# Performance work log

Measured on AMD Instinct MI355X. Metric: run time of the kernel, lower is better.

The kernel has to match this reference:

```python
import jax, jax.numpy as jnp
import numpy as np

B, N, F_DIM, HID, HEADS = 4, 1024, 512, 64, 8  # feature_dim == HID*HEADS required by the module's += broadcast


def setup_inputs() -> dict:
    key = jax.random.key(0)
    ks = jax.random.split(key, 16)
    s = 0.05
    return {
        'node_features_a': jax.random.normal(ks[0], (B, N, F_DIM), dtype=jnp.float32),
        'node_features_b': jax.random.normal(ks[1], (B, N, F_DIM), dtype=jnp.float32),
        'A_intra_a': jax.random.uniform(ks[2], (B, N, N), dtype=jnp.float32),
        'A_intra_b': jax.random.uniform(ks[3], (B, N, N), dtype=jnp.float32),
        'A_inter': jax.random.uniform(ks[4], (B, N, N), dtype=jnp.float32),
        # stacked per-head Linear weights (torch ModuleList F1/F2/F3), [H, F, K]
        'W1': jax.random.normal(ks[5], (HEADS, F_DIM, HID), dtype=jnp.float32) * s,
        'b1': jnp.zeros((HEADS, HID), jnp.float32),
        'W2': jax.random.normal(ks[6], (HEADS, F_DIM, HID), dtype=jnp.float32) * s,
        'b2': jnp.zeros((HEADS, HID), jnp.float32),
        'W3': jax.random.normal(ks[7], (HEADS, F_DIM, HID), dtype=jnp.float32) * s,
        'b3': jnp.zeros((HEADS, HID), jnp.float32),
        'W_intra_a': jax.random.normal(ks[8], (HID, HID), dtype=jnp.float32) * s,
        'W_intra_b': jax.random.normal(ks[9], (HID, HID), dtype=jnp.float32) * s,
        'W_inter': jax.random.normal(ks[10], (HID, HID), dtype=jnp.float32) * s,
        'W_out': jax.random.normal(ks[11], (F_DIM, HID * HEADS), dtype=jnp.float32) * s,  # torch Linear weight [out,in]
        'b_out': jnp.zeros((F_DIM,), jnp.float32),
        'b_output': jnp.zeros((F_DIM,), jnp.float32),
    }


def _aggregate(src, tgt, adj, ew, W1, b1, W2, b2, W3, b3, W_out, b_out, b_output):
    # per-head projections, batched over heads instead of a Python loop
    F1u = jnp.einsum('bnf,hfk->bhnk', src, W1) + b1[:, None, :]
    F2v = jnp.einsum('bmf,hfk->bhmk', tgt, W2) + b2[:, None, :]
    F3u = jnp.einsum('bnf,hfk->bhnk', src, W3) + b3[:, None, :]
    # attention_scores = F1_u @ (edge_weight @ F2_v^T)  -> [B,H,N,N]
    scores = jnp.einsum('bhnk,kl,bhml->bhnm', F1u, ew, F2v)
    # multiplicative adjacency mask, then softmax over last dim
    attn = jax.nn.softmax(scores * adj[:, None, :, :], axis=-1)
    msgs = jnp.einsum('bhnm,bhmk->bhnk', attn, F3u)
    b_, h_, n_, k_ = msgs.shape
    concat = msgs.transpose(0, 2, 1, 3).reshape(b_, n_, h_ * k_)  # cat heads on last dim
    return jax.nn.relu(concat @ W_out.T + b_out) + b_output


def reference(node_features_a, node_features_b, A_intra_a, A_intra_b, A_inter,
              W1, b1, W2, b2, W3, b3, W_intra_a, W_intra_b, W_inter,
              W_out, b_out, b_output):
    p = (W1, b1, W2, b2, W3, b3)
    o = (W_out, b_out, b_output)
    ua = _aggregate(node_features_a, node_features_a, A_intra_a, W_intra_a, *p, *o)
    ub = _aggregate(node_features_b, node_features_b, A_intra_b, W_intra_b, *p, *o)
    ia = _aggregate(node_features_a, node_features_b, A_inter, W_inter, *p, *o)
    ib = _aggregate(node_features_b, node_features_a, jnp.swapaxes(A_inter, 1, 2), W_inter, *p, *o)
    return (ua + ia, ub + ib)
```

## Files before the change

kernel.cpp:

```cpp
#include <hip/hip_runtime.h>
#include <hip/hip_bf16.h>

#define BB 4
#define NN 1024
#define FF 512
#define HH 8
#define KK 64
#define PSZ ((size_t)BB * HH * NN * KK)

#define XAOFF 0u
#define XBOFF 2097152u
#define WTOFF 4194304u
#define WOOFF (WTOFF + 786432u)
#define PBOFF (WOOFF + 262144u)
#define MSOFF (PBOFF + 6u * 2097152u)
#define ADOFF (MSOFF + 4u * 2097152u)
#define ADSZ  4194304u

#define LOG2E 1.4426950408889634f
#define SHIFT2 34.624683f

typedef unsigned short u16;
typedef __attribute__((ext_vector_type(8))) short bf16x8;
typedef __attribute__((ext_vector_type(4))) short bf16x4;
typedef __attribute__((ext_vector_type(4))) float f32x4;
typedef __attribute__((ext_vector_type(8))) unsigned short ushort8;
typedef __attribute__((ext_vector_type(4))) unsigned short ushort4v;

#if defined(__has_builtin)
#if __has_builtin(__builtin_amdgcn_mfma_f32_16x16x16bf16_1k)
#define HAVE_MFMA16 1
#endif
#if __has_builtin(__builtin_amdgcn_global_load_lds)
#define HAVE_GLL 1
#endif
#endif
#ifndef HAVE_MFMA16
#define HAVE_MFMA16 0
#endif
#ifndef HAVE_GLL
#define HAVE_GLL 0
#endif

#if HAVE_GLL
#define GSTR 64
#else
#define GSTR 72
#endif

__device__ __forceinline__ u16 f2b(float x) {
    union { float f; unsigned u; } v; v.f = x;
    unsigned r = v.u + 0x7FFF + ((v.u >> 16) & 1);
    return (u16)(r >> 16);
}
__device__ __forceinline__ float b2f(u16 x) {
    union { unsigned u; float f; } v; v.u = ((unsigned)x) << 16;
    return v.f;
}

__global__ __launch_bounds__(256) void prep_kernel(
    const float* __restrict__ Xa, const float* __restrict__ Xb,
    const float* __restrict__ Wout,
    const float* __restrict__ W1, const float* __restrict__ W2,
    const float* __restrict__ W3,
    u16* __restrict__ ws)
{
    __shared__ float T[64][65];
    const int bid = blockIdx.x;
    const int t = threadIdx.x;

    if (bid < 192) {
        const int j  = bid / 64;
        const int rem = bid & 63;
        const int h  = rem >> 3;
        const int f0 = (rem & 7) * 64;
        const float* Wj = j == 0 ? W1 : (j == 1 ? W2 : W3);
        const int tr = t >> 2, tc = (t & 3) * 16;
        const float* src = Wj + (size_t)h * FF * KK + (size_t)(f0 + tr) * KK + tc;
        #pragma unroll
        for (int jj = 0; jj < 4; ++jj) {
            float4 v = *(const float4*)(src + 4 * jj);
            T[tr][tc + 4 * jj + 0] = v.x;
            T[tr][tc + 4 * jj + 1] = v.y;
            T[tr][tc + 4 * jj + 2] = v.z;
            T[tr][tc + 4 * jj + 3] = v.w;
        }
        __syncthreads();
        ushort8 w0, w1;
        #pragma unroll
        for (int jj = 0; jj < 8; ++jj) {
            w0[jj] = f2b(T[tc + jj][tr]);
            w1[jj] = f2b(T[tc + 8 + jj][tr]);
        }
        u16* d = ws + WTOFF + (unsigned)j * 262144u + (unsigned)(h * 64 + tr) * 512u + f0 + tc;
        *(ushort8*)&d[0] = w0;
        *(ushort8*)&d[8] = w1;
        return;
    }

    const int NFLAT4 = (2097152 + 2097152 + 262144) / 4;
    const int nb = gridDim.x - 192;
    for (int idx = (bid - 192) * 256 + t; idx < NFLAT4; idx += nb * 256) {
        int e = idx * 4;
        const float* src; u16* dst;
        if (e < 2097152)      { src = Xa + e;             dst = ws + XAOFF + e; }
        else if (e < 4194304) { src = Xb + (e - 2097152); dst = ws + XBOFF + (e - 2097152); }
        else                  { src = Wout + (e - 4194304); dst = ws + WOOFF + (e - 4194304); }
        float4 v = *(const float4*)src;
        ushort4v w;
        w[0] = f2b(v.x); w[1] = f2b(v.y); w[2] = f2b(v.z); w[3] = f2b(v.w);
        *(ushort4v*)dst = w;
    }
}

__global__ __launch_bounds__(256) void perm_kernel(
    const float* __restrict__ Aia, const float* __restrict__ Aib,
    const float* __restrict__ Ain, u16* __restrict__ ws)
{
    const int z = blockIdx.z;
    const int b = blockIdx.y;
    const int x = blockIdx.x;
    const int qblk = x >> 4, mt = x & 15;
    const float* A = (z == 0 ? Aia : (z == 1 ? Aib : Ain)) + ((size_t)b << 20);
    u16* out = ws + ADOFF + (size_t)z * ADSZ + ((size_t)b << 20) + (size_t)x * 8192;
    const int t = threadIdx.x;
    const int w = t >> 6, l = t & 63;
    const int lg = l >> 4, li = l & 15;
    #pragma unroll
    for (int u = 0; u < 2; ++u)
        #pragma unroll
        for (int t_ = 0; t_ < 4; ++t_) {
            const int row = qblk * 128 + w * 32 + u * 16 + li;
            const int col = mt * 64 + t_ * 16 + lg * 4;
            float4 v = *(const float4*)&A[(size_t)row * NN + col];
            ushort4v o;
            o[0] = f2b(v.x * LOG2E); o[1] = f2b(v.y * LOG2E);
            o[2] = f2b(v.z * LOG2E); o[3] = f2b(v.w * LOG2E);
            *(ushort4v*)&out[(size_t)(w * 8 + u * 4 + t_) * 256 + l * 4] = o;
        }
}

__global__ __launch_bounds__(256) void permt_kernel(const float* __restrict__ Ain, u16* __restrict__ dst)
{
    const int b = blockIdx.y;
    const int x = blockIdx.x;
    const int qblk = x >> 4, mt = x & 15;
    __shared__ float T[64][132];
    const int t = threadIdx.x;
    const int tr = t >> 2, tc = (t & 3) * 32;
    const float* src = Ain + ((size_t)b << 20) + (size_t)(mt * 64 + tr) * NN + qblk * 128 + tc;
    #pragma unroll
    for (int j = 0; j < 8; ++j) {
        float4 v = *(const float4*)(src + 4 * j);
        T[tr][tc + 4 * j + 0] = v.x;
        T[tr][tc + 4 * j + 1] = v.y;
        T[tr][tc + 4 * j + 2] = v.z;
        T[tr][tc + 4 * j + 3] = v.w;
    }
    __syncthreads();
    const int w = t >> 6, l = t & 63;
    const int lg = l >> 4, li = l & 15;
    u16* out = dst + ((size_t)b << 20) + (size_t)x * 8192;
    #pragma unroll
    for (int u = 0; u < 2; ++u)
        #pragma unroll
        for (int t_ = 0; t_ < 4; ++t_) {
            ushort4v o;
            #pragma unroll
            for (int e = 0; e < 4; ++e)
                o[e] = f2b(T[t_ * 16 + lg * 4 + e][w * 32 + u * 16 + li] * LOG2E);
            *(ushort4v*)&out[(size_t)(w * 8 + u * 4 + t_) * 256 + l * 4] = o;
        }
}

__global__ __launch_bounds__(256) void proj_kernel(
    const float* __restrict__ b1v, const float* __restrict__ b2v,
    const float* __restrict__ b3v,
    u16* __restrict__ ws)
{
    const int z  = blockIdx.z;
    const int src = z / 3, pj = z % 3;
    const u16* X  = ws + (src ? XBOFF : XAOFF);
    const u16* Wt = ws + WTOFF + (unsigned)pj * 262144u;
    const float* bias = pj == 0 ? b1v : (pj == 1 ? b2v : b3v);
    u16* P = ws + PBOFF + (size_t)z * PSZ;

    const int rb = blockIdx.y * 128;
    const int cb = blockIdx.x * 128;
    const int t  = threadIdx.x;
    const int lane = t & 63, wave = t >> 6;
    const int lg = lane >> 4, li = lane & 15;
    const int wr = wave >> 1, wc = wave & 1;

    __shared__ u16 As[128 * GSTR];
    __shared__ u16 Bs[128 * GSTR];

    f32x4 acc[4][4];
    #pragma unroll
    for (int m = 0; m < 4; ++m)
        #pragma unroll
        for (int n = 0; n < 4; ++n) acc[m][n] = (f32x4){0.f, 0.f, 0.f, 0.f};

#if !HAVE_GLL
    const int srow = t >> 1, sf0 = (t & 1) * 32;
#endif

    for (int fb = 0; fb < FF; fb += 64) {
        __syncthreads();
#if HAVE_GLL
        {
            const int gr = wave * 32 + (lane >> 3);
            const int gc = (lane & 7) * 8;
            #pragma unroll
            for (int i = 0; i < 4; ++i) {
                __builtin_amdgcn_global_load_lds(
                    (const unsigned int*)&X[(size_t)(rb + gr + 8 * i) * FF + fb + gc],
                    (unsigned int*)&As[(wave * 32 + 8 * i) * GSTR], 16, 0, 0);
                __builtin_amdgcn_global_load_lds(
                    (const unsigned int*)&Wt[(size_t)(cb + gr + 8 * i) * FF + fb + gc],
                    (unsigned int*)&Bs[(wave * 32 + 8 * i) * GSTR], 16, 0, 0);
            }
        }
#else
        #pragma unroll
        for (int s = 0; s < 4; ++s) {
            *(ushort8*)&As[srow * GSTR + sf0 + 8 * s] =
                *(const ushort8*)&X[(size_t)(rb + srow) * FF + fb + sf0 + 8 * s];
            *(ushort8*)&Bs[srow * GSTR + sf0 + 8 * s] =
                *(const ushort8*)&Wt[(size_t)(cb + srow) * FF + fb + sf0 + 8 * s];
        }
#endif
        __syncthreads();

        bf16x8 af[4][2], bf[4][2];
        #pragma unroll
        for (int m = 0; m < 4; ++m) {
            af[m][0] = *(const bf16x8*)&As[(wr * 64 + m * 16 + li) * GSTR + 8 * lg];
            af[m][1] = *(const bf16x8*)&As[(wr * 64 + m * 16 + li) * GSTR + 8 * lg + 32];
        }
        #pragma unroll
        for (int n = 0; n < 4; ++n) {
            bf[n][0] = *(const bf16x8*)&Bs[(wc * 64 + n * 16 + li) * GSTR + 8 * lg];
            bf[n][1] = *(const bf16x8*)&Bs[(wc * 64 + n * 16 + li) * GSTR + 8 * lg + 32];
        }
        #pragma unroll
        for (int m = 0; m < 4; ++m)
            #pragma unroll
            for (int n = 0; n < 4; ++n) {
                acc[m][n] = __builtin_amdgcn_mfma_f32_16x16x32_bf16(af[m][0], bf[n][0], acc[m][n], 0, 0, 0);
                acc[m][n] = __builtin_amdgcn_mfma_f32_16x16x32_bf16(af[m][1], bf[n][1], acc[m][n], 0, 0, 0);
            }
    }

    if (pj != 2) {
        #pragma unroll
        for (int m = 0; m < 4; ++m)
            #pragma unroll
            for (int n = 0; n < 4; ++n)
                #pragma unroll
                for (int r = 0; r < 4; ++r) {
                    int row = rb + wr * 64 + m * 16 + 4 * lg + r;
                    int col = cb + wc * 64 + n * 16 + li;
                    int b_ = row >> 10, n_ = row & 1023;
                    int h = col >> 6, k = col & 63;
                    P[((size_t)(b_ * HH + h) * NN + n_) * KK + k] = f2b(acc[m][n][r] + bias[col]);
                }
    } else {
        #pragma unroll
        for (int m = 0; m < 4; ++m)
            #pragma unroll
            for (int n = 0; n < 4; ++n) {
                int col = cb + wc * 64 + n * 16 + li;
                int h = col >> 6, k = col & 63;
                int row0 = rb + wr * 64 + m * 16 + 4 * lg;
                int b_ = row0 >> 10, n0 = row0 & 1023;
                float bsv = bias[col];
                ushort4v w;
                #pragma unroll
                for (int r = 0; r < 4; ++r) w[r] = f2b(acc[m][n][r] + bsv);
                *(ushort4v*)&P[((size_t)(b_ * HH + h) * KK + k) * NN + n0] = w;
            }
    }
}

#define SWU(ROW, CU) (((ROW) << 6) + ((CU) ^ (((ROW) & 7) << 3)))

__global__ __launch_bounds__(256, 4) void attn_kernel(
    const u16* __restrict__ Pbase,
    const float* __restrict__ Wia, const float* __restrict__ Wib, const float* __restrict__ Win,
    const u16* __restrict__ AD, const u16* __restrict__ AinT,
    u16* __restrict__ msgs)
{
    const int flat = blockIdx.x;
    const int lf   = (flat & 7) * 128 + (flat >> 3);
    const int qblk = lf & 7;
    const int qb   = qblk * 128;
    const int bh   = (lf >> 3) & 31;
    const int agg  = lf >> 8;
    const int b = bh >> 3, h = bh & 7;
    const int t = threadIdx.x;
    const int lane = t & 63, wave = t >> 6;
    const int lg = lane >> 4, li = lane & 15;

    const u16 *Qp, *Kp, *Vp, *adjp; const float* ew;
    switch (agg) {
      case 0: Qp = Pbase;         ew = Wia; Kp = Pbase + 1*PSZ; Vp = Pbase + 2*PSZ; adjp = AD;          break;
      case 1: Qp = Pbase + 3*PSZ; ew = Wib; Kp = Pbase + 4*PSZ; Vp = Pbase + 5*PSZ; adjp = AD + 1*ADSZ; break;
      case 2: Qp = Pbase;         ew = Win; Kp = Pbase + 4*PSZ; Vp = Pbase + 2*PSZ; adjp = AD + 2*ADSZ; break;
      default:Qp = Pbase + 3*PSZ; ew = Win; Kp = Pbase + 1*PSZ; Vp = Pbase + 5*PSZ; adjp = AinT;        break;
    }
    const size_t bhoff = (size_t)(b * HH + h) * NN * KK;
    const u16* Qbh  = Qp + bhoff;
    const u16* Kbh  = Kp + bhoff;
    const u16* Vbh  = Vp + bhoff;
    const u16* advs = adjp + ((size_t)b << 20) + (size_t)qblk * 131072u
                           + (unsigned)(wave * 2048 + lane * 4);

    __shared__ u16 SM[16384];
    u16* preQ = SM;
    u16* preF = SM + 8192;
    u16* preE = SM + 12288;

    const int sr  = t >> 2;
    const int sc  = (t & 3) * 16;

    #pragma unroll
    for (int j = 0; j < 16; ++j)
        preE[SWU(sc + j, sr)] = f2b(ew[sr * 64 + sc + j]);

    #pragma unroll
    for (int p = 0; p < 2; ++p) {
        __syncthreads();
        {
            const ushort8* src = (const ushort8*)&Qbh[(size_t)(qb + p * 64 + sr) * KK + sc];
            *(ushort8*)&preF[SWU(sr, sc)]     = src[0];
            *(ushort8*)&preF[SWU(sr, sc + 8)] = src[1];
        }
        __syncthreads();
        bf16x8 a0 = *(const bf16x8*)&preF[SWU(wave * 16 + li, 8 * lg)];
        bf16x8 a1 = *(const bf16x8*)&preF[SWU(wave * 16 + li, 8 * lg + 32)];
        #pragma unroll
        for (int t_ = 0; t_ < 4; ++t_) {
            bf16x8 b0 = *(const bf16x8*)&preE[SWU(li + 16 * t_, 8 * lg)];
            bf16x8 b1 = *(const bf16x8*)&preE[SWU(li + 16 * t_, 8 * lg + 32)];
            f32x4 q = {0.f, 0.f, 0.f, 0.f};
            q = __builtin_amdgcn_mfma_f32_16x16x32_bf16(a0, b0, q, 0, 0, 0);
            q = __builtin_amdgcn_mfma_f32_16x16x32_bf16(a1, b1, q, 0, 0, 0);
            #pragma unroll
            for (int r = 0; r < 4; ++r)
                preQ[SWU(p * 64 + wave * 16 + 4 * lg + r, li + 16 * t_)] = f2b(q[r]);
        }
    }
    __syncthreads();
    bf16x8 qB[2][2];
    #pragma unroll
    for (int u = 0; u < 2; ++u)
        #pragma unroll
        for (int c = 0; c < 2; ++c)
            qB[u][c] = *(const bf16x8*)&preQ[SWU(wave * 32 + u * 16 + li, 32 * c + 8 * lg)];
    __syncthreads();

    f32x4 oacc[2][4];
    #pragma unroll
    for (int u = 0; u < 2; ++u)
        #pragma unroll
        for (int f_ = 0; f_ < 4; ++f_) oacc[u][f_] = (f32x4){0.f, 0.f, 0.f, 0.f};
    float lsum[2] = {0.f, 0.f};

#if HAVE_MFMA16
    {
        const ushort8* ks = (const ushort8*)&Kbh[(size_t)sr * KK + sc];
        *(ushort8*)&SM[SWU(sr, sc)]            = ks[0];
        *(ushort8*)&SM[SWU(sr, sc + 8)]        = ks[1];
        const ushort8* vs = (const ushort8*)&Vbh[(size_t)sr * NN + sc];
        *(ushort8*)&SM[8192 + SWU(sr, sc)]     = vs[0];
        *(ushort8*)&SM[8192 + SWU(sr, sc + 8)] = vs[1];
    }
    __syncthreads();

    for (int mt = 0; mt < 16; ++mt) {
        const int cur = (mt & 1) * 4096;
        const u16* Kc = SM + cur;
        const u16* Vc = SM + 8192 + cur;

        ushort8 kr0, kr1, vr0, vr1;
        if (mt < 15) {
            const int mb2 = (mt + 1) * 64;
            const ushort8* ks = (const ushort8*)&Kbh[(size_t)(mb2 + sr) * KK + sc];
            kr0 = ks[0]; kr1 = ks[1];
            const ushort8* vs = (const ushort8*)&Vbh[(size_t)sr * NN + mb2 + sc];
            vr0 = vs[0]; vr1 = vs[1];
        }

        ushort4v adv[2][4];
        {
            const u16* ap = advs + (size_t)mt * 8192;
            #pragma unroll
            for (int u = 0; u < 2; ++u)
                #pragma unroll
                for (int t_ = 0; t_ < 4; ++t_)
                    adv[u][t_] = *(const ushort4v*)&ap[(u * 4 + t_) * 256];
        }

        bf16x4 pa[2][4];
        #pragma unroll
        for (int t_ = 0; t_ < 4; ++t_) {
            bf16x8 kb0 = *(const bf16x8*)&Kc[SWU(li + 16 * t_, 8 * lg)];
            bf16x8 kb1 = *(const bf16x8*)&Kc[SWU(li + 16 * t_, 8 * lg + 32)];
            #pragma unroll
            for (int u = 0; u < 2; ++u) {
                f32x4 s = {0.f, 0.f, 0.f, 0.f};
                __builtin_amdgcn_s_setprio(1);
                s = __builtin_amdgcn_mfma_f32_16x16x32_bf16(kb0, qB[u][0], s, 0, 0, 0);
                s = __builtin_amdgcn_mfma_f32_16x16x32_bf16(kb1, qB[u][1], s, 0, 0, 0);
                __builtin_amdgcn_s_setprio(0);
                float p0 = __builtin_amdgcn_exp2f(fmaf(s[0], b2f(adv[u][t_][0]), -SHIFT2));
                float p1 = __builtin_amdgcn_exp2f(fmaf(s[1], b2f(adv[u][t_][1]), -SHIFT2));
                float p2 = __builtin_amdgcn_exp2f(fmaf(s[2], b2f(adv[u][t_][2]), -SHIFT2));
                float p3 = __builtin_amdgcn_exp2f(fmaf(s[3], b2f(adv[u][t_][3]), -SHIFT2));
                lsum[u] += (p0 + p1) + (p2 + p3);
                unsigned w0, w1;
                asm("v_cvt_pk_bf16_f32 %0, %1, %2" : "=v"(w0) : "v"(p0), "v"(p1));
                asm("v_cvt_pk_bf16_f32 %0, %1, %2" : "=v"(w1) : "v"(p2), "v"(p3));
                union { uint2 u2; bf16x4 v; } pk;
                pk.u2.x = w0; pk.u2.y = w1;
                pa[u][t_] = pk.v;
            }
        }

        __builtin_amdgcn_s_setprio(1);
        #pragma unroll
        for (int f_ = 0; f_ < 4; ++f_) {
            #pragma unroll
            for (int t_ = 0; t_ < 4; ++t_) {
                bf16x4 vb = *(const bf16x4*)&Vc[SWU(li + 16 * f_, 16 * t_ + 4 * lg)];
                oacc[0][f_] = __builtin_amdgcn_mfma_f32_16x16x16bf16_1k(pa[0][t_], vb, oacc[0][f_], 0, 0, 0);
                oacc[1][f_] = __builtin_amdgcn_mfma_f32_16x16x16bf16_1k(pa[1][t_], vb, oacc[1][f_], 0, 0, 0);
            }
        }
        __builtin_amdgcn_s_setprio(0);

        if (mt < 15) {
            const int nxt = ((mt & 1) ^ 1) * 4096;
            *(ushort8*)&SM[nxt + SWU(sr, sc)]            = kr0;
            *(ushort8*)&SM[nxt + SWU(sr, sc + 8)]        = kr1;
            *(ushort8*)&SM[8192 + nxt + SWU(sr, sc)]     = vr0;
            *(ushort8*)&SM[8192 + nxt + SWU(sr, sc + 8)] = vr1;
        }
        __syncthreads();
    }
#else
    u16* Kt = SM;
    u16* Vt = SM + 4096;
    u16* Pq = SM + 8192;
    for (int mt = 0; mt < 16; ++mt) {
        const int mb = mt * 64;
        __syncthreads();
        {
            const ushort8* ks = (const ushort8*)&Kbh[(size_t)(mb + sr) * KK + sc];
            *(ushort8*)&Kt[SWU(sr, sc)]     = ks[0];
            *(ushort8*)&Kt[SWU(sr, sc + 8)] = ks[1];
            const ushort8* vs = (const ushort8*)&Vbh[(size_t)sr * NN + mb + sc];
            *(ushort8*)&Vt[SWU(sr, sc)]     = vs[0];
            *(ushort8*)&Vt[SWU(sr, sc + 8)] = vs[1];
        }
        __syncthreads();

        ushort4v adv[2][4];
        {
            const u16* ap = advs + (size_t)mt * 8192;
            #pragma unroll
            for (int u = 0; u < 2; ++u)
                #pragma unroll
                for (int t_ = 0; t_ < 4; ++t_)
                    adv[u][t_] = *(const ushort4v*)&ap[(u * 4 + t_) * 256];
        }

        #pragma unroll
        for (int t_ = 0; t_ < 4; ++t_) {
            bf16x8 kb0 = *(const bf16x8*)&Kt[SWU(li + 16 * t_, 8 * lg)];
            bf16x8 kb1 = *(const bf16x8*)&Kt[SWU(li + 16 * t_, 8 * lg + 32)];
            #pragma unroll
            for (int u = 0; u < 2; ++u) {
                f32x4 s = {0.f, 0.f, 0.f, 0.f};
                s = __builtin_amdgcn_mfma_f32_16x16x32_bf16(kb0, qB[u][0], s, 0, 0, 0);
                s = __builtin_amdgcn_mfma_f32_16x16x32_bf16(kb1, qB[u][1], s, 0, 0, 0);
                float p0 = __builtin_amdgcn_exp2f(fmaf(s[0], b2f(adv[u][t_][0]), -SHIFT2));
                float p1 = __builtin_amdgcn_exp2f(fmaf(s[1], b2f(adv[u][t_][1]), -SHIFT2));
                float p2 = __builtin_amdgcn_exp2f(fmaf(s[2], b2f(adv[u][t_][2]), -SHIFT2));
                float p3 = __builtin_amdgcn_exp2f(fmaf(s[3], b2f(adv[u][t_][3]), -SHIFT2));
                lsum[u] += (p0 + p1) + (p2 + p3);
                unsigned w0, w1;
                asm("v_cvt_pk_bf16_f32 %0, %1, %2" : "=v"(w0) : "v"(p0), "v"(p1));
                asm("v_cvt_pk_bf16_f32 %0, %1, %2" : "=v"(w1) : "v"(p2), "v"(p3));
                uint2 pd; pd.x = w0; pd.y = w1;
                *(uint2*)&Pq[SWU(wave * 32 + u * 16 + li, 16 * t_ + 4 * lg)] = pd;
            }
        }
        {
            bf16x8 pA[2][2];
            #pragma unroll
            for (int u = 0; u < 2; ++u) {
                pA[u][0] = *(const bf16x8*)&Pq[SWU(wave * 32 + u * 16 + li, 8 * lg)];
                pA[u][1] = *(const bf16x8*)&Pq[SWU(wave * 32 + u * 16 + li, 8 * lg + 32)];
            }
            #pragma unroll
            for (int f_ = 0; f_ < 4; ++f_) {
                bf16x8 vb0 = *(const bf16x8*)&Vt[SWU(li + 16 * f_, 8 * lg)];
                bf16x8 vb1 = *(const bf16x8*)&Vt[SWU(li + 16 * f_, 8 * lg + 32)];
                #pragma unroll
                for (int u = 0; u < 2; ++u) {
                    oacc[u][f_] = __builtin_amdgcn_mfma_f32_16x16x32_bf16(pA[u][0], vb0, oacc[u][f_], 0, 0, 0);
                    oacc[u][f_] = __builtin_amdgcn_mfma_f32_16x16x32_bf16(pA[u][1], vb1, oacc[u][f_], 0, 0, 0);
                }
            }
        }
    }
#endif

    #pragma unroll
    for (int u = 0; u < 2; ++u) {
        lsum[u] += __shfl_xor(lsum[u], 16);
        lsum[u] += __shfl_xor(lsum[u], 32);
    }
    #pragma unroll
    for (int u = 0; u < 2; ++u)
        #pragma unroll
        for (int r = 0; r < 4; ++r) {
            float inv = 1.f / __shfl(lsum[u], 4 * lg + r);
            int row = qb + wave * 32 + u * 16 + 4 * lg + r;
            u16* dst = msgs + (size_t)agg * PSZ + ((size_t)b * NN + row) * (HH * KK) + h * KK;
            #pragma unroll
            for (int f_ = 0; f_ < 4; ++f_)
                dst[li + 16 * f_] = f2b(oacc[u][f_][r] * inv);
        }
}

__global__ __launch_bounds__(256) void out_kernel(
    const u16* __restrict__ ws,
    const float* __restrict__ bo, const float* __restrict__ bo2,
    float* __restrict__ out)
{
    const int z  = blockIdx.z;
    const u16* M1 = ws + MSOFF + (size_t)z * PSZ;
    const u16* M2 = ws + MSOFF + (size_t)(2 + z) * PSZ;
    const u16* Wb = ws + WOOFF;
    const int rb = blockIdx.y * 64;
    const int cb = blockIdx.x * 128;
    const int t  = threadIdx.x;
    const int lane = t & 63, wave = t >> 6;
    const int lg = lane >> 4, li = lane & 15;
    const int wr = wave >> 1, wc = wave & 1;

    __shared__ u16 A1s[64 * GSTR];
    __shared__ u16 A2s[64 * GSTR];
    __shared__ u16 Bs[128 * GSTR];

    f32x4 acc1[2][4], acc2[2][4];
    #pragma unroll
    for (int m = 0; m < 2; ++m)
        #pragma unroll
        for (int n = 0; n < 4; ++n) {
            acc1[m][n] = (f32x4){0.f, 0.f, 0.f, 0.f};
            acc2[m][n] = (f32x4){0.f, 0.f, 0.f, 0.f};
        }

    for (int fb = 0; fb < FF; fb += 64) {
        __syncthreads();
#if HAVE_GLL
        {
            const int lr = lane >> 3;
            const int gc = (lane & 7) * 8;
            #pragma unroll
            for (int i = 0; i < 2; ++i) {
                __builtin_amdgcn_global_load_lds(
                    (const unsigned int*)&M1[(size_t)(rb + wave * 16 + 8 * i + lr) * FF + fb + gc],
                    (unsigned int*)&A1s[(wave * 16 + 8 * i) * GSTR], 16, 0, 0);
                __builtin_amdgcn_global_load_lds(
                    (const unsigned int*)&M2[(size_t)(rb + wave * 16 + 8 * i + lr) * FF + fb + gc],
                    (unsigned int*)&A2s[(wave * 16 + 8 * i) * GSTR], 16, 0, 0);
            }
            #pragma unroll
            for (int i = 0; i < 4; ++i) {
                __builtin_amdgcn_global_load_lds(
                    (const unsigned int*)&Wb[(size_t)(cb + wave * 32 + 8 * i + lr) * FF + fb + gc],
                    (unsigned int*)&Bs[(wave * 32 + 8 * i) * GSTR], 16, 0, 0);
            }
        }
#else
        {
            int ar = t >> 2, ac = (t & 3) * 16;
            *(ushort8*)&A1s[ar * GSTR + ac]     = *(const ushort8*)&M1[(size_t)(rb + ar) * FF + fb + ac];
            *(ushort8*)&A1s[ar * GSTR + ac + 8] = *(const ushort8*)&M1[(size_t)(rb + ar) * FF + fb + ac + 8];
            *(ushort8*)&A2s[ar * GSTR + ac]     = *(const ushort8*)&M2[(size_t)(rb + ar) * FF + fb + ac];
            *(ushort8*)&A2s[ar * GSTR + ac + 8] = *(const ushort8*)&M2[(size_t)(rb + ar) * FF + fb + ac + 8];
            int br = t >> 1, bc = (t & 1) * 32;
            #pragma unroll
            for (int s = 0; s < 4; ++s)
                *(ushort8*)&Bs[br * GSTR + bc + 8 * s] =
                    *(const ushort8*)&Wb[(size_t)(cb + br) * FF + fb + bc + 8 * s];
        }
#endif
        __syncthreads();

        #pragma unroll
        for (int m = 0; m < 2; ++m) {
            bf16x8 a10 = *(const bf16x8*)&A1s[(wr * 32 + m * 16 + li) * GSTR + 8 * lg];
            bf16x8 a11 = *(const bf16x8*)&A1s[(wr * 32 + m * 16 + li) * GSTR + 8 * lg + 32];
            bf16x8 a20 = *(const bf16x8*)&A2s[(wr * 32 + m * 16 + li) * GSTR + 8 * lg];
            bf16x8 a21 = *(const bf16x8*)&A2s[(wr * 32 + m * 16 + li) * GSTR + 8 * lg + 32];
            #pragma unroll
            for (int n = 0; n < 4; ++n) {
                bf16x8 b0 = *(const bf16x8*)&Bs[(wc * 64 + n * 16 + li) * GSTR + 8 * lg];
                bf16x8 b1 = *(const bf16x8*)&Bs[(wc * 64 + n * 16 + li) * GSTR + 8 * lg + 32];
                acc1[m][n] = __builtin_amdgcn_mfma_f32_16x16x32_bf16(a10, b0, acc1[m][n], 0, 0, 0);
                acc1[m][n] = __builtin_amdgcn_mfma_f32_16x16x32_bf16(a11, b1, acc1[m][n], 0, 0, 0);
                acc2[m][n] = __builtin_amdgcn_mfma_f32_16x16x32_bf16(a20, b0, acc2[m][n], 0, 0, 0);
                acc2[m][n] = __builtin_amdgcn_mfma_f32_16x16x32_bf16(a21, b1, acc2[m][n], 0, 0, 0);
            }
        }
    }

    #pragma unroll
    for (int m = 0; m < 2; ++m)
        #pragma unroll
        for (int n = 0; n < 4; ++n)
            #pragma unroll
            for (int r = 0; r < 4; ++r) {
                int row = rb + wr * 32 + m * 16 + 4 * lg + r;
                int col = cb + wc * 64 + n * 16 + li;
                float v1 = fmaxf(acc1[m][n][r] + bo[col], 0.f);
                float v2 = fmaxf(acc2[m][n][r] + bo[col], 0.f);
                out[(size_t)z * (BB * NN * FF) + (size_t)row * FF + col] = v1 + v2 + 2.f * bo2[col];
            }
}

extern "C" void kernel_launch(void* const* d_in, const int* in_sizes, int n_in,
                              void* d_out, int out_size, void* d_ws, size_t ws_size,
                              hipStream_t stream) {
    const float* nfa  = (const float*)d_in[0];
    const float* nfb  = (const float*)d_in[1];
    const float* Aia  = (const float*)d_in[2];
    const float* Aib  = (const float*)d_in[3];
    const float* Ain  = (const float*)d_in[4];
    const float* W1   = (const float*)d_in[5];
    const float* b1   = (const float*)d_in[6];
    const float* W2   = (const float*)d_in[7];
    const float* b2   = (const float*)d_in[8];
    const float* W3   = (const float*)d_in[9];
    const float* b3   = (const float*)d_in[10];
    const float* Wia  = (const float*)d_in[11];
    const float* Wib  = (const float*)d_in[12];
    const float* Win  = (const float*)d_in[13];
    const float* Wout = (const float*)d_in[14];
    const float* bo   = (const float*)d_in[15];
    const float* bo2  = (const float*)d_in[16];

    u16* ws = (u16*)d_ws;
    float* out = (float*)d_out;

    prep_kernel<<<1536, 256, 0, stream>>>(nfa, nfb, Wout, W1, W2, W3, ws);
    perm_kernel<<<dim3(128, 4, 3), 256, 0, stream>>>(Aia, Aib, Ain, ws);
    proj_kernel<<<dim3(4, 32, 6), 256, 0, stream>>>(b1, b2, b3, ws);
    permt_kernel<<<dim3(128, 4), 256, 0, stream>>>(Ain, ws + XAOFF);
    attn_kernel<<<1024, 256, 0, stream>>>(ws + PBOFF, Wia, Wib, Win, ws + ADOFF, ws + XAOFF, ws + MSOFF);
    out_kernel<<<dim3(4, 64, 2), 256, 0, stream>>>(ws, bo, bo2, out);
}
```

Measured before the change: 133.6 us.

## Split attention key dimension across wave pairs and stage K/V via global_load_lds

```diff
diff --git a/kernel.cpp b/kernel.cpp
--- a/kernel.cpp
+++ b/kernel.cpp
@@ -285,7 +285,7 @@
 
 #define SWU(ROW, CU) (((ROW) << 6) + ((CU) ^ (((ROW) & 7) << 3)))
 
-__global__ __launch_bounds__(256, 4) void attn_kernel(
+__global__ __launch_bounds__(512, 6) void attn_kernel(
     const u16* __restrict__ Pbase,
     const float* __restrict__ Wia, const float* __restrict__ Wib, const float* __restrict__ Win,
     const u16* __restrict__ AD, const u16* __restrict__ AinT,
@@ -301,6 +301,7 @@
     const int t = threadIdx.x;
     const int lane = t & 63, wave = t >> 6;
     const int lg = lane >> 4, li = lane & 15;
+    const int qg = wave >> 1, mh = wave & 1;
 
     const u16 *Qp, *Kp, *Vp, *adjp; const float* ew;
     switch (agg) {
@@ -314,31 +315,30 @@
     const u16* Kbh  = Kp + bhoff;
     const u16* Vbh  = Vp + bhoff;
     const u16* advs = adjp + ((size_t)b << 20) + (size_t)qblk * 131072u
-                           + (unsigned)(wave * 2048 + lane * 4);
+                           + (unsigned)((qg * 8 + mh * 2) * 256 + lane * 4);
 
     __shared__ u16 SM[16384];
-    u16* preQ = SM;
-    u16* preF = SM + 8192;
-    u16* preE = SM + 12288;
-
-    const int sr  = t >> 2;
-    const int sc  = (t & 3) * 16;
-
-    #pragma unroll
-    for (int j = 0; j < 16; ++j)
-        preE[SWU(sc + j, sr)] = f2b(ew[sr * 64 + sc + j]);
-
-    #pragma unroll
-    for (int p = 0; p < 2; ++p) {
-        __syncthreads();
-        {
-            const ushort8* src = (const ushort8*)&Qbh[(size_t)(qb + p * 64 + sr) * KK + sc];
-            *(ushort8*)&preF[SWU(sr, sc)]     = src[0];
-            *(ushort8*)&preF[SWU(sr, sc + 8)] = src[1];
-        }
-        __syncthreads();
-        bf16x8 a0 = *(const bf16x8*)&preF[SWU(wave * 16 + li, 8 * lg)];
-        bf16x8 a1 = *(const bf16x8*)&preF[SWU(wave * 16 + li, 8 * lg + 32)];
+    char* SMc = (char*)SM;
+    u16* Qs   = SM;
+    u16* preE = SM + 8192;
+
+    {
+        const int sr3 = t >> 3, sc3 = (t & 7) * 8;
+        #pragma unroll
+        for (int j = 0; j < 8; ++j)
+            preE[SWU(sc3 + j, sr3)] = f2b(ew[sr3 * 64 + sc3 + j]);
+    }
+    {
+        const int qr = t >> 2, qc = (t & 3) * 16;
+        const ushort8* src = (const ushort8*)&Qbh[(size_t)(qb + qr) * KK + qc];
+        *(ushort8*)&Qs[SWU(qr, qc)]     = src[0];
+        *(ushort8*)&Qs[SWU(qr, qc + 8)] = src[1];
+    }
+    __syncthreads();
+    f32x4 qreg[4];
+    {
+        bf16x8 a0 = *(const bf16x8*)&Qs[SWU(wave * 16 + li, 8 * lg)];
+        bf16x8 a1 = *(const bf16x8*)&Qs[SWU(wave * 16 + li, 8 * lg + 32)];
         #pragma unroll
         for (int t_ = 0; t_ < 4; ++t_) {
             bf16x8 b0 = *(const bf16x8*)&preE[SWU(li + 16 * t_, 8 * lg)];
@@ -346,18 +346,22 @@
             f32x4 q = {0.f, 0.f, 0.f, 0.f};
             q = __builtin_amdgcn_mfma_f32_16x16x32_bf16(a0, b0, q, 0, 0, 0);
             q = __builtin_amdgcn_mfma_f32_16x16x32_bf16(a1, b1, q, 0, 0, 0);
-            #pragma unroll
-            for (int r = 0; r < 4; ++r)
-                preQ[SWU(p * 64 + wave * 16 + 4 * lg + r, li + 16 * t_)] = f2b(q[r]);
-        }
-    }
+            qreg[t_] = q;
+        }
+    }
+    __syncthreads();
+    #pragma unroll
+    for (int t_ = 0; t_ < 4; ++t_)
+        #pragma unroll
+        for (int r = 0; r < 4; ++r)
+            Qs[SWU(wave * 16 + 4 * lg + r, li + 16 * t_)] = f2b(qreg[t_][r]);
     __syncthreads();
     bf16x8 qB[2][2];
     #pragma unroll
     for (int u = 0; u < 2; ++u)
         #pragma unroll
         for (int c = 0; c < 2; ++c)
-            qB[u][c] = *(const bf16x8*)&preQ[SWU(wave * 32 + u * 16 + li, 32 * c + 8 * lg)];
+            qB[u][c] = *(const bf16x8*)&Qs[SWU(qg * 32 + u * 16 + li, 32 * c + 8 * lg)];
     __syncthreads();
 
     f32x4 oacc[2][4];
@@ -367,44 +371,47 @@
         for (int f_ = 0; f_ < 4; ++f_) oacc[u][f_] = (f32x4){0.f, 0.f, 0.f, 0.f};
     float lsum[2] = {0.f, 0.f};
 
-#if HAVE_MFMA16
-    {
-        const ushort8* ks = (const ushort8*)&Kbh[(size_t)sr * KK + sc];
-        *(ushort8*)&SM[SWU(sr, sc)]            = ks[0];
-        *(ushort8*)&SM[SWU(sr, sc + 8)]        = ks[1];
-        const ushort8* vs = (const ushort8*)&Vbh[(size_t)sr * NN + sc];
-        *(ushort8*)&SM[8192 + SWU(sr, sc)]     = vs[0];
-        *(ushort8*)&SM[8192 + SWU(sr, sc + 8)] = vs[1];
-    }
+#if HAVE_MFMA16 && HAVE_GLL
+    const int lrow = lane >> 3;
+    const int lcs  = ((lane & 7) ^ lrow) * 8;
+
+    __builtin_amdgcn_global_load_lds(
+        (const unsigned int*)&Kbh[(size_t)(wave * 8 + lrow) * KK + lcs],
+        (unsigned int*)(SMc + wave * 1024), 16, 0, 0);
+    __builtin_amdgcn_global_load_lds(
+        (const unsigned int*)&Vbh[(size_t)(wave * 8 + lrow) * NN + lcs],
+        (unsigned int*)(SMc + 16384 + wave * 1024), 16, 0, 0);
     __syncthreads();
 
     for (int mt = 0; mt < 16; ++mt) {
-        const int cur = (mt & 1) * 4096;
-        const u16* Kc = SM + cur;
-        const u16* Vc = SM + 8192 + cur;
-
-        ushort8 kr0, kr1, vr0, vr1;
+        const u16* Kc = (const u16*)(SMc + (mt & 1) * 8192);
+        const u16* Vc = (const u16*)(SMc + 16384 + (mt & 1) * 8192);
+
         if (mt < 15) {
             const int mb2 = (mt + 1) * 64;
-            const ushort8* ks = (const ushort8*)&Kbh[(size_t)(mb2 + sr) * KK + sc];
-            kr0 = ks[0]; kr1 = ks[1];
-            const ushort8* vs = (const ushort8*)&Vbh[(size_t)sr * NN + mb2 + sc];
-            vr0 = vs[0]; vr1 = vs[1];
-        }
-
-        ushort4v adv[2][4];
+            const int nb  = ((mt & 1) ^ 1) * 8192;
+            __builtin_amdgcn_global_load_lds(
+                (const unsigned int*)&Kbh[(size_t)(mb2 + wave * 8 + lrow) * KK + lcs],
+                (unsigned int*)(SMc + nb + wave * 1024), 16, 0, 0);
+            __builtin_amdgcn_global_load_lds(
+                (const unsigned int*)&Vbh[(size_t)(wave * 8 + lrow) * NN + mb2 + lcs],
+                (unsigned int*)(SMc + 16384 + nb + wave * 1024), 16, 0, 0);
+        }
+
+        ushort4v adv[2][2];
         {
             const u16* ap = advs + (size_t)mt * 8192;
             #pragma unroll
             for (int u = 0; u < 2; ++u)
                 #pragma unroll
-                for (int t_ = 0; t_ < 4; ++t_)
-                    adv[u][t_] = *(const ushort4v*)&ap[(u * 4 + t_) * 256];
-        }
-
-        bf16x4 pa[2][4];
-        #pragma unroll
-        for (int t_ = 0; t_ < 4; ++t_) {
+                for (int tt = 0; tt < 2; ++tt)
+                    adv[u][tt] = *(const ushort4v*)&ap[(u * 4 + tt) * 256];
+        }
+
+        bf16x4 pa[2][2];
+        #pragma unroll
+        for (int tt = 0; tt < 2; ++tt) {
+            const int t_ = mh * 2 + tt;
             bf16x8 kb0 = *(const bf16x8*)&Kc[SWU(li + 16 * t_, 8 * lg)];
             bf16x8 kb1 = *(const bf16x8*)&Kc[SWU(li + 16 * t_, 8 * lg + 32)];
             #pragma unroll
@@ -414,17 +421,17 @@
                 s = __builtin_amdgcn_mfma_f32_16x16x32_bf16(kb0, qB[u][0], s, 0, 0, 0);
                 s = __builtin_amdgcn_mfma_f32_16x16x32_bf16(kb1, qB[u][1], s, 0, 0, 0);
                 __builtin_amdgcn_s_setprio(0);
-                float p0 = __builtin_amdgcn_exp2f(fmaf(s[0], b2f(adv[u][t_][0]), -SHIFT2));
-                float p1 = __builtin_amdgcn_exp2f(fmaf(s[1], b2f(adv[u][t_][1]), -SHIFT2));
-                float p2 = __builtin_amdgcn_exp2f(fmaf(s[2], b2f(adv[u][t_][2]), -SHIFT2));
-                float p3 = __builtin_amdgcn_exp2f(fmaf(s[3], b2f(adv[u][t_][3]), -SHIFT2));
+                float p0 = __builtin_amdgcn_exp2f(fmaf(s[0], b2f(adv[u][tt][0]), -SHIFT2));
+                float p1 = __builtin_amdgcn_exp2f(fmaf(s[1], b2f(adv[u][tt][1]), -SHIFT2));
+                float p2 = __builtin_amdgcn_exp2f(fmaf(s[2], b2f(adv[u][tt][2]), -SHIFT2));
+                float p3 = __builtin_amdgcn_exp2f(fmaf(s[3], b2f(adv[u][tt][3]), -SHIFT2));
                 lsum[u] += (p0 + p1) + (p2 + p3);
                 unsigned w0, w1;
                 asm("v_cvt_pk_bf16_f32 %0, %1, %2" : "=v"(w0) : "v"(p0), "v"(p1));
                 asm("v_cvt_pk_bf16_f32 %0, %1, %2" : "=v"(w1) : "v"(p2), "v"(p3));
                 union { uint2 u2; bf16x4 v; } pk;
                 pk.u2.x = w0; pk.u2.y = w1;
-                pa[u][t_] = pk.v;
+                pa[u][tt] = pk.v;
             }
         }
 
@@ -432,77 +439,108 @@
         #pragma unroll
         for (int f_ = 0; f_ < 4; ++f_) {
             #pragma unroll
-            for (int t_ = 0; t_ < 4; ++t_) {
+            for (int tt = 0; tt < 2; ++tt) {
+                const int t_ = mh * 2 + tt;
                 bf16x4 vb = *(const bf16x4*)&Vc[SWU(li + 16 * f_, 16 * t_ + 4 * lg)];
-                oacc[0][f_] = __builtin_amdgcn_mfma_f32_16x16x16bf16_1k(pa[0][t_], vb, oacc[0][f_], 0, 0, 0);
-                oacc[1][f_] = __builtin_amdgcn_mfma_f32_16x16x16bf16_1k(pa[1][t_], vb, oacc[1][f_], 0, 0, 0);
+                oacc[0][f_] = __builtin_amdgcn_mfma_f32_16x16x16bf16_1k(pa[0][tt], vb, oacc[0][f_], 0, 0, 0);
+                oacc[1][f_] = __builtin_amdgcn_mfma_f32_16x16x16bf16_1k(pa[1][tt], vb, oacc[1][f_], 0, 0, 0);
             }
         }
         __builtin_amdgcn_s_setprio(0);
 
-        if (mt < 15) {
-            const int nxt = ((mt & 1) ^ 1) * 4096;
-            *(ushort8*)&SM[nxt + SWU(sr, sc)]            = kr0;
-            *(ushort8*)&SM[nxt + SWU(sr, sc + 8)]        = kr1;
-            *(ushort8*)&SM[8192 + nxt + SWU(sr, sc)]     = vr0;
-            *(ushort8*)&SM[8192 + nxt + SWU(sr, sc + 8)] = vr1;
-        }
         __syncthreads();
+    }
+
+    #pragma unroll
+    for (int u = 0; u < 2; ++u) {
+        lsum[u] += __shfl_xor(lsum[u], 16);
+        lsum[u] += __shfl_xor(lsum[u], 32);
+    }
+    float* SMf = (float*)SM;
+    if (lg == 0) {
+        SMf[wave * 32 + li]      = lsum[0];
+        SMf[wave * 32 + 16 + li] = lsum[1];
+    }
+    __syncthreads();
+    #pragma unroll
+    for (int u = 0; u < 2; ++u)
+        lsum[u] = SMf[wave * 32 + u * 16 + li] + SMf[(wave ^ 1) * 32 + u * 16 + li];
+    __syncthreads();
+    if (mh == 0) {
+        #pragma unroll
+        for (int u = 0; u < 2; ++u)
+            #pragma unroll
+            for (int f_ = 0; f_ < 4; ++f_)
+                #pragma unroll
+                for (int r = 0; r < 4; ++r)
+                    SMf[qg * 2048 + (u * 16 + 4 * lg + r) * 64 + li + 16 * f_] = oacc[u][f_][r];
+    }
+    __syncthreads();
+    if (mh == 1) {
+        #pragma unroll
+        for (int u = 0; u < 2; ++u)
+            #pragma unroll
+            for (int r = 0; r < 4; ++r) {
+                float inv = 1.f / __shfl(lsum[u], 4 * lg + r);
+                int row = qb + qg * 32 + u * 16 + 4 * lg + r;
+                u16* dst = msgs + (size_t)agg * PSZ + ((size_t)b * NN + row) * (HH * KK) + h * KK;
+                #pragma unroll
+                for (int f_ = 0; f_ < 4; ++f_) {
+                    float v = oacc[u][f_][r]
+                            + SMf[qg * 2048 + (u * 16 + 4 * lg + r) * 64 + li + 16 * f_];
+                    dst[li + 16 * f_] = f2b(v * inv);
+                }
+            }
     }
 #else
     u16* Kt = SM;
     u16* Vt = SM + 4096;
     u16* Pq = SM + 8192;
+    const u16* apf = adjp + ((size_t)b << 20) + (size_t)qblk * 131072u
+                          + (unsigned)(qg * 8 * 256 + lane * 4);
     for (int mt = 0; mt < 16; ++mt) {
         const int mb = mt * 64;
         __syncthreads();
         {
-            const ushort8* ks = (const ushort8*)&Kbh[(size_t)(mb + sr) * KK + sc];
-            *(ushort8*)&Kt[SWU(sr, sc)]     = ks[0];
-            *(ushort8*)&Kt[SWU(sr, sc + 8)] = ks[1];
-            const ushort8* vs = (const ushort8*)&Vbh[(size_t)sr * NN + mb + sc];
-            *(ushort8*)&Vt[SWU(sr, sc)]     = vs[0];
-            *(ushort8*)&Vt[SWU(sr, sc + 8)] = vs[1];
+            const int kr = t >> 3, kc = (t & 7) * 8;
+            *(ushort8*)&Kt[SWU(kr, kc)] = *(const ushort8*)&Kbh[(size_t)(mb + kr) * KK + kc];
+            *(ushort8*)&Vt[SWU(kr, kc)] = *(const ushort8*)&Vbh[(size_t)kr * NN + mb + kc];
         }
         __syncthreads();
-
-        ushort4v adv[2][4];
-        {
-            const u16* ap = advs + (size_t)mt * 8192;
+        if (mh == 0) {
+            ushort4v adv[2][4];
+            const u16* ap = apf + (size_t)mt * 8192;
             #pragma unroll
             for (int u = 0; u < 2; ++u)
                 #pragma unroll
                 for (int t_ = 0; t_ < 4; ++t_)
                     adv[u][t_] = *(const ushort4v*)&ap[(u * 4 + t_) * 256];
-        }
-
-        #pragma unroll
-        for (int t_ = 0; t_ < 4; ++t_) {
-            bf16x8 kb0 = *(const bf16x8*)&Kt[SWU(li + 16 * t_, 8 * lg)];
-            bf16x8 kb1 = *(const bf16x8*)&Kt[SWU(li + 16 * t_, 8 * lg + 32)];
+            #pragma unroll
+            for (int t_ = 0; t_ < 4; ++t_) {
+                bf16x8 kb0 = *(const bf16x8*)&Kt[SWU(li + 16 * t_, 8 * lg)];
+                bf16x8 kb1 = *(const bf16x8*)&Kt[SWU(li + 16 * t_, 8 * lg + 32)];
+                #pragma unroll
+                for (int u = 0; u < 2; ++u) {
+                    f32x4 s = {0.f, 0.f, 0.f, 0.f};
+                    s = __builtin_amdgcn_mfma_f32_16x16x32_bf16(kb0, qB[u][0], s, 0, 0, 0);
+                    s = __builtin_amdgcn_mfma_f32_16x16x32_bf16(kb1, qB[u][1], s, 0, 0, 0);
+                    float p0 = __builtin_amdgcn_exp2f(fmaf(s[0], b2f(adv[u][t_][0]), -SHIFT2));
+                    float p1 = __builtin_amdgcn_exp2f(fmaf(s[1], b2f(adv[u][t_][1]), -SHIFT2));
+                    float p2 = __builtin_amdgcn_exp2f(fmaf(s[2], b2f(adv[u][t_][2]), -SHIFT2));
+                    float p3 = __builtin_amdgcn_exp2f(fmaf(s[3], b2f(adv[u][t_][3]), -SHIFT2));
+                    lsum[u] += (p0 + p1) + (p2 + p3);
+                    unsigned w0, w1;
+                    asm("v_cvt_pk_bf16_f32 %0, %1, %2" : "=v"(w0) : "v"(p0), "v"(p1));
+                    asm("v_cvt_pk_bf16_f32 %0, %1, %2" : "=v"(w1) : "v"(p2), "v"(p3));
+                    uint2 pd; pd.x = w0; pd.y = w1;
+                    *(uint2*)&Pq[SWU(qg * 32 + u * 16 + li, 16 * t_ + 4 * lg)] = pd;
+                }
+            }
+            bf16x8 pA[2][2];
             #pragma unroll
             for (int u = 0; u < 2; ++u) {
-                f32x4 s = {0.f, 0.f, 0.f, 0.f};
-                s = __builtin_amdgcn_mfma_f32_16x16x32_bf16(kb0, qB[u][0], s, 0, 0, 0);
-                s = __builtin_amdgcn_mfma_f32_16x16x32_bf16(kb1, qB[u][1], s, 0, 0, 0);
-                float p0 = __builtin_amdgcn_exp2f(fmaf(s[0], b2f(adv[u][t_][0]), -SHIFT2));
-                float p1 = __builtin_amdgcn_exp2f(fmaf(s[1], b2f(adv[u][t_][1]), -SHIFT2));
-                float p2 = __builtin_amdgcn_exp2f(fmaf(s[2], b2f(adv[u][t_][2]), -SHIFT2));
-                float p3 = __builtin_amdgcn_exp2f(fmaf(s[3], b2f(adv[u][t_][3]), -SHIFT2));
-                lsum[u] += (p0 + p1) + (p2 + p3);
-                unsigned w0, w1;
-                asm("v_cvt_pk_bf16_f32 %0, %1, %2" : "=v"(w0) : "v"(p0), "v"(p1));
-                asm("v_cvt_pk_bf16_f32 %0, %1, %2" : "=v"(w1) : "v"(p2), "v"(p3));
-                uint2 pd; pd.x = w0; pd.y = w1;
-                *(uint2*)&Pq[SWU(wave * 32 + u * 16 + li, 16 * t_ + 4 * lg)] = pd;
-            }
-        }
-        {
-            bf16x8 pA[2][2];
-            #pragma unroll
-            for (int u = 0; u < 2; ++u) {
-                pA[u][0] = *(const bf16x8*)&Pq[SWU(wave * 32 + u * 16 + li, 8 * lg)];
-                pA[u][1] = *(const bf16x8*)&Pq[SWU(wave * 32 + u * 16 + li, 8 * lg + 32)];
+                pA[u][0] = *(const bf16x8*)&Pq[SWU(qg * 32 + u * 16 + li, 8 * lg)];
+                pA[u][1] = *(const bf16x8*)&Pq[SWU(qg * 32 + u * 16 + li, 8 * lg + 32)];
             }
             #pragma unroll
             for (int f_ = 0; f_ < 4; ++f_) {
@@ -516,24 +554,25 @@
             }
         }
     }
-#endif
-
     #pragma unroll
     for (int u = 0; u < 2; ++u) {
         lsum[u] += __shfl_xor(lsum[u], 16);
         lsum[u] += __shfl_xor(lsum[u], 32);
     }
-    #pragma unroll
-    for (int u = 0; u < 2; ++u)
-        #pragma unroll
-        for (int r = 0; r < 4; ++r) {
-            float inv = 1.f / __shfl(lsum[u], 4 * lg + r);
-            int row = qb + wave * 32 + u * 16 + 4 * lg + r;
-            u16* dst = msgs + (size_t)agg * PSZ + ((size_t)b * NN + row) * (HH * KK) + h * KK;
-            #pragma unroll
-            for (int f_ = 0; f_ < 4; ++f_)
-                dst[li + 16 * f_] = f2b(oacc[u][f_][r] * inv);
-        }
+    if (mh == 0) {
+        #pragma unroll
+        for (int u = 0; u < 2; ++u)
+            #pragma unroll
+            for (int r = 0; r < 4; ++r) {
+                float inv = 1.f / __shfl(lsum[u], 4 * lg + r);
+                int row = qb + qg * 32 + u * 16 + 4 * lg + r;
+                u16* dst = msgs + (size_t)agg * PSZ + ((size_t)b * NN + row) * (HH * KK) + h * KK;
+                #pragma unroll
+                for (int f_ = 0; f_ < 4; ++f_)
+                    dst[li + 16 * f_] = f2b(oacc[u][f_][r] * inv);
+            }
+    }
+#endif
 }
 
 __global__ __launch_bounds__(256) void out_kernel(
@@ -663,6 +702,6 @@
     perm_kernel<<<dim3(128, 4, 3), 256, 0, stream>>>(Aia, Aib, Ain, ws);
     proj_kernel<<<dim3(4, 32, 6), 256, 0, stream>>>(b1, b2, b3, ws);
     permt_kernel<<<dim3(128, 4), 256, 0, stream>>>(Ain, ws + XAOFF);
-    attn_kernel<<<1024, 256, 0, stream>>>(ws + PBOFF, Wia, Wib, Win, ws + ADOFF, ws + XAOFF, ws + MSOFF);
+    attn_kernel<<<1024, 512, 0, stream>>>(ws + PBOFF, Wia, Wib, Win, ws + ADOFF, ws + XAOFF, ws + MSOFF);
     out_kernel<<<dim3(4, 64, 2), 256, 0, stream>>>(ws, bo, bo2, out);
 }
```

After: 305.4 us. 129% more time.
